# Performance work log

Hardware: AMD Instinct MI355X
Metric: run time of the kernel (lower is better)

Reference implementation:

```python
import jax, jax.numpy as jnp
import numpy as np

N_HEAD = 12
HEAD_DIM = 64
N_EMBD = 768
ATTN_MULT = 0.125
B, T = 2, 2048
NEG_INF = -1e30


def setup_inputs() -> dict:
    key = jax.random.key(0)
    ks = jax.random.split(key, 3)
    x = jax.random.normal(ks[0], (B, T, N_EMBD), dtype=jnp.float32)
    W_attn = jax.random.normal(ks[1], (N_EMBD, 3 * N_HEAD * HEAD_DIM), dtype=jnp.float32) * 0.02
    b_attn = jnp.zeros((3 * N_HEAD * HEAD_DIM,), dtype=jnp.float32)
    W_proj = jax.random.normal(ks[2], (N_HEAD * HEAD_DIM, N_EMBD), dtype=jnp.float32) * 0.02
    b_proj = jnp.zeros((N_EMBD,), dtype=jnp.float32)
    return {"x": x, "W_attn": W_attn, "b_attn": b_attn, "W_proj": W_proj, "b_proj": b_proj}


def reference(x, W_attn, b_attn, W_proj, b_proj):
    Bsz, Tlen, C = x.shape
    H, D = N_HEAD, HEAD_DIM
    qkv = x @ W_attn + b_attn                       # [B,T,3*H*D]
    q, k, v = jnp.split(qkv, 3, axis=-1)
    q = q.reshape(Bsz, Tlen, H, D).transpose(0, 2, 1, 3)   # [B,H,T,D]
    k = k.reshape(Bsz, Tlen, H, D).transpose(0, 2, 1, 3)
    v = v.reshape(Bsz, Tlen, H, D).transpose(0, 2, 1, 3)

    att = jnp.einsum('bhtd,bhsd->bhts', q, k) * ATTN_MULT  # [B,H,T,T]
    causal = jnp.tril(jnp.ones((Tlen, Tlen), dtype=bool))  # [T,T]
    att = jnp.where(causal, att, NEG_INF)

    # selection mask from head 0 (SelectionHeadLinearComboKind.NONE)
    S = jax.nn.relu(att[:, 0:1, :, :])                     # [B,1,T,T]; relu kills -inf
    # protect_bos_token: zero column 0 (key index 0)
    col = jnp.arange(Tlen)
    S = S * (col[None, None, None, :] != 0)
    # prevent_from_masking_myself: zero diagonal
    S = S * (1.0 - jnp.eye(Tlen, dtype=S.dtype))

    # accumulate selection over query (row) axis: ProtectionKind.NONE
    FF = jnp.cumsum(S, axis=-2)                            # [B,1,T,T]
    att = att - FF                                         # broadcast over heads

    p = jax.nn.softmax(att, axis=-1)                       # [B,H,T,T]
    y = jnp.einsum('bhts,bhsd->bhtd', p, v)                # [B,H,T,D]
    y = y.transpose(0, 2, 1, 3).reshape(Bsz, Tlen, H * D)  # [B,T,H*D]
    return y @ W_proj + b_proj
```

## Files before the change

### kernel.cpp

```cpp
#include <hip/hip_runtime.h>
#include <math.h>

#define T 2048
#define NH 12
#define HD 64
#define C3 2304
#define CE 768
#define NB 2

typedef __attribute__((ext_vector_type(8))) short bf16x8;
typedef __attribute__((ext_vector_type(4))) float f32x4;
typedef __attribute__((ext_vector_type(16))) float f32x16;
typedef __attribute__((ext_vector_type(4))) unsigned u32x4;

__device__ __forceinline__ void gload16(const void* g, void* l) {
    __builtin_amdgcn_global_load_lds(
        (const __attribute__((address_space(1))) void*)g,
        (__attribute__((address_space(3))) void*)l, 16, 0, 0);
}

__device__ inline void bf16split(float a, unsigned short& h, unsigned short& l) {
    unsigned int u = __float_as_uint(a);
    unsigned int r = (u + 0x7FFFu + ((u >> 16) & 1u)) >> 16;
    h = (unsigned short)r;
    float hf = __uint_as_float(r << 16);
    float lo = a - hf;
    unsigned int v = __float_as_uint(lo);
    l = (unsigned short)((v + 0x7FFFu + ((v >> 16) & 1u)) >> 16);
}

__device__ inline void packPfast(float a, float b, unsigned& wh, unsigned& wl) {
    unsigned ua = __float_as_uint(a), ub = __float_as_uint(b);
    unsigned ha = ua >> 16, hb = ub & 0xFFFF0000u;
    float la = a - __uint_as_float(ha << 16);
    float lb = b - __uint_as_float(hb);
    wh = ha | hb;
    wl = (__float_as_uint(la) >> 16) | (__float_as_uint(lb) & 0xFFFF0000u);
}

__global__ __launch_bounds__(256) void cvt_split_kernel(const float* __restrict__ A,
        unsigned short* __restrict__ H, unsigned short* __restrict__ L) {
    int i = blockIdx.x * 256 + threadIdx.x;
    float4 a0 = *(reinterpret_cast<const float4*>(A) + (size_t)i * 2);
    float4 a1 = *(reinterpret_cast<const float4*>(A) + (size_t)i * 2 + 1);
    float f[8] = {a0.x, a0.y, a0.z, a0.w, a1.x, a1.y, a1.z, a1.w};
    unsigned short h[8], l[8];
    #pragma unroll
    for (int j = 0; j < 8; ++j) bf16split(f[j], h[j], l[j]);
    uint4 hv, lv;
    hv.x = (unsigned)h[0] | ((unsigned)h[1] << 16); hv.y = (unsigned)h[2] | ((unsigned)h[3] << 16);
    hv.z = (unsigned)h[4] | ((unsigned)h[5] << 16); hv.w = (unsigned)h[6] | ((unsigned)h[7] << 16);
    lv.x = (unsigned)l[0] | ((unsigned)l[1] << 16); lv.y = (unsigned)l[2] | ((unsigned)l[3] << 16);
    lv.z = (unsigned)l[4] | ((unsigned)l[5] << 16); lv.w = (unsigned)l[6] | ((unsigned)l[7] << 16);
    reinterpret_cast<uint4*>(H)[i] = hv;
    reinterpret_cast<uint4*>(L)[i] = lv;
}

__global__ __launch_bounds__(256) void cvt_split_T_kernel(const float* __restrict__ W,
        unsigned short* __restrict__ H, unsigned short* __restrict__ L, int K, int N) {
    __shared__ float tile[64][65];
    const int n0 = blockIdx.x * 64, k0 = blockIdx.y * 64;
    const int t = threadIdx.x;
    {
        int r = t >> 2, c4 = (t & 3) * 16;
        #pragma unroll
        for (int u = 0; u < 4; ++u) {
            float4 w = *reinterpret_cast<const float4*>(&W[(size_t)(k0 + r) * N + n0 + c4 + u * 4]);
            tile[r][c4 + u * 4 + 0] = w.x; tile[r][c4 + u * 4 + 1] = w.y;
            tile[r][c4 + u * 4 + 2] = w.z; tile[r][c4 + u * 4 + 3] = w.w;
        }
    }
    __syncthreads();
    {
        int n = t >> 2, kc = (t & 3) * 16;
        unsigned short h[16], l[16];
        #pragma unroll
        for (int j = 0; j < 16; ++j) bf16split(tile[kc + j][n], h[j], l[j]);
        uint4 hv0, hv1, lv0, lv1;
        hv0.x = (unsigned)h[0] | ((unsigned)h[1] << 16);  hv0.y = (unsigned)h[2] | ((unsigned)h[3] << 16);
        hv0.z = (unsigned)h[4] | ((unsigned)h[5] << 16);  hv0.w = (unsigned)h[6] | ((unsigned)h[7] << 16);
        hv1.x = (unsigned)h[8] | ((unsigned)h[9] << 16);  hv1.y = (unsigned)h[10] | ((unsigned)h[11] << 16);
        hv1.z = (unsigned)h[12] | ((unsigned)h[13] << 16); hv1.w = (unsigned)h[14] | ((unsigned)h[15] << 16);
        lv0.x = (unsigned)l[0] | ((unsigned)l[1] << 16);  lv0.y = (unsigned)l[2] | ((unsigned)l[3] << 16);
        lv0.z = (unsigned)l[4] | ((unsigned)l[5] << 16);  lv0.w = (unsigned)l[6] | ((unsigned)l[7] << 16);
        lv1.x = (unsigned)l[8] | ((unsigned)l[9] << 16);  lv1.y = (unsigned)l[10] | ((unsigned)l[11] << 16);
        lv1.z = (unsigned)l[12] | ((unsigned)l[13] << 16); lv1.w = (unsigned)l[14] | ((unsigned)l[15] << 16);
        size_t o = (size_t)(n0 + n) * K + k0 + kc;
        reinterpret_cast<uint4*>(&H[o])[0] = hv0; reinterpret_cast<uint4*>(&H[o])[1] = hv1;
        reinterpret_cast<uint4*>(&L[o])[0] = lv0; reinterpret_cast<uint4*>(&L[o])[1] = lv1;
    }
}

__global__ __launch_bounds__(256) void cvt_kv_vt_kernel(const float* __restrict__ Vtmp,
        unsigned short* __restrict__ Vh, unsigned short* __restrict__ Vl) {
    __shared__ float tile[64][65];
    const int s0 = blockIdx.x * 64;
    const int bh = blockIdx.y;
    const int tid = threadIdx.x;
    {
        int r = tid >> 2, c0 = (tid & 3) * 16;
        const float* src = Vtmp + ((size_t)bh * T + s0 + r) * 64 + c0;
        #pragma unroll
        for (int u = 0; u < 4; ++u) {
            float4 w = *reinterpret_cast<const float4*>(src + u * 4);
            tile[r][c0 + u * 4 + 0] = w.x; tile[r][c0 + u * 4 + 1] = w.y;
            tile[r][c0 + u * 4 + 2] = w.z; tile[r][c0 + u * 4 + 3] = w.w;
        }
    }
    __syncthreads();
    {
        int d = tid >> 2, cs = (tid & 3) * 16;
        unsigned short hh[16], ll[16];
        #pragma unroll
        for (int j = 0; j < 16; ++j) bf16split(tile[cs + j][d], hh[j], ll[j]);
        uint4 hv0, hv1, lv0, lv1;
        hv0.x = (unsigned)hh[0] | ((unsigned)hh[1] << 16);  hv0.y = (unsigned)hh[2] | ((unsigned)hh[3] << 16);
        hv0.z = (unsigned)hh[4] | ((unsigned)hh[5] << 16);  hv0.w = (unsigned)hh[6] | ((unsigned)hh[7] << 16);
        hv1.x = (unsigned)hh[8] | ((unsigned)hh[9] << 16);  hv1.y = (unsigned)hh[10] | ((unsigned)hh[11] << 16);
        hv1.z = (unsigned)hh[12] | ((unsigned)hh[13] << 16); hv1.w = (unsigned)hh[14] | ((unsigned)hh[15] << 16);
        lv0.x = (unsigned)ll[0] | ((unsigned)ll[1] << 16);  lv0.y = (unsigned)ll[2] | ((unsigned)ll[3] << 16);
        lv0.z = (unsigned)ll[4] | ((unsigned)ll[5] << 16);  lv0.w = (unsigned)ll[6] | ((unsigned)ll[7] << 16);
        lv1.x = (unsigned)ll[8] | ((unsigned)ll[9] << 16);  lv1.y = (unsigned)ll[10] | ((unsigned)ll[11] << 16);
        lv1.z = (unsigned)ll[12] | ((unsigned)ll[13] << 16); lv1.w = (unsigned)ll[14] | ((unsigned)ll[15] << 16);
        size_t o = ((size_t)bh * 64 + d) * T + s0 + cs;
        reinterpret_cast<uint4*>(&Vh[o])[0] = hv0; reinterpret_cast<uint4*>(&Vh[o])[1] = hv1;
        reinterpret_cast<uint4*>(&Vl[o])[0] = lv0; reinterpret_cast<uint4*>(&Vl[o])[1] = lv1;
    }
}

#define LD32 32
__global__ __launch_bounds__(256) void gemm_mfma_kernel(
        const unsigned short* __restrict__ Ah, const unsigned short* __restrict__ Al,
        const unsigned short* __restrict__ Bh, const unsigned short* __restrict__ Bl,
        const float* __restrict__ bias, float* __restrict__ Cm,
        int M, int N, int K) {
    __shared__ unsigned short lA[2][128 * LD32];
    __shared__ unsigned short lB[2][128 * LD32];
    const int tid = threadIdx.x;
    const int nwg = gridDim.x * gridDim.y;
    int bid = blockIdx.y * gridDim.x + blockIdx.x;
    bid = (bid & 7) * (nwg >> 3) + (bid >> 3);
    const int bm = (bid / gridDim.x) * 128, bn = (bid % gridDim.x) * 128;
    const int lane = tid & 63, wid = tid >> 6;
    const int wr = wid >> 1, wc = wid & 1;
    f32x4 acc[4][4];
    #pragma unroll
    for (int i = 0; i < 4; ++i)
        #pragma unroll
        for (int j = 0; j < 4; ++j) acc[i][j] = (f32x4){0.f, 0.f, 0.f, 0.f};
    const int srow0 = wid * 32 + (lane >> 2);
    const int scn   = lane & 3;
    const int arb = wr * 64 + (lane & 15);
    const int brb = wc * 64 + (lane & 15);
    const int kc  = lane >> 4;
    for (int k0 = 0; k0 < K; k0 += 32) {
        __syncthreads();
        #pragma unroll
        for (int h = 0; h < 2; ++h) {
            int row = srow0 + h * 16;
            int cs = scn ^ ((row >> 1) & 3);
            size_t ao = (size_t)(bm + row) * K + k0 + cs * 8;
            size_t bo = (size_t)(bn + row) * K + k0 + cs * 8;
            unsigned short* d0 = &lA[0][(wid * 32 + h * 16) * LD32];
            unsigned short* d1 = &lA[1][(wid * 32 + h * 16) * LD32];
            unsigned short* d2 = &lB[0][(wid * 32 + h * 16) * LD32];
            unsigned short* d3 = &lB[1][(wid * 32 + h * 16) * LD32];
            gload16(&Ah[ao], d0);
            gload16(&Al[ao], d1);
            gload16(&Bh[bo], d2);
            gload16(&Bl[bo], d3);
        }
        __syncthreads();
        bf16x8 fa[2][4], fb[2][4];
        #pragma unroll
        for (int fi = 0; fi < 4; ++fi) {
            int ra = arb + fi * 16, rb = brb + fi * 16;
            int ca = (kc ^ ((ra >> 1) & 3)) * 8;
            int cb = (kc ^ ((rb >> 1) & 3)) * 8;
            fa[0][fi] = *reinterpret_cast<const bf16x8*>(&lA[0][ra * LD32 + ca]);
            fa[1][fi] = *reinterpret_cast<const bf16x8*>(&lA[1][ra * LD32 + ca]);
            fb[0][fi] = *reinterpret_cast<const bf16x8*>(&lB[0][rb * LD32 + cb]);
            fb[1][fi] = *reinterpret_cast<const bf16x8*>(&lB[1][rb * LD32 + cb]);
        }
        #pragma unroll
        for (int fi = 0; fi < 4; ++fi)
            #pragma unroll
            for (int fj = 0; fj < 4; ++fj) {
                acc[fi][fj] = __builtin_amdgcn_mfma_f32_16x16x32_bf16(fb[0][fj], fa[0][fi], acc[fi][fj], 0, 0, 0);
                acc[fi][fj] = __builtin_amdgcn_mfma_f32_16x16x32_bf16(fb[0][fj], fa[1][fi], acc[fi][fj], 0, 0, 0);
                acc[fi][fj] = __builtin_amdgcn_mfma_f32_16x16x32_bf16(fb[1][fj], fa[0][fi], acc[fi][fj], 0, 0, 0);
            }
    }
    const int mloc = lane & 15, ng = (lane >> 4) * 4;
    #pragma unroll
    for (int fi = 0; fi < 4; ++fi) {
        int row = bm + wr * 64 + fi * 16 + mloc;
        #pragma unroll
        for (int fj = 0; fj < 4; ++fj) {
            int n0 = bn + wc * 64 + fj * 16 + ng;
            float4 bv = *reinterpret_cast<const float4*>(&bias[n0]);
            float4 o4 = {acc[fi][fj][0] + bv.x, acc[fi][fj][1] + bv.y,
                         acc[fi][fj][2] + bv.z, acc[fi][fj][3] + bv.w};
            *reinterpret_cast<float4*>(&Cm[(size_t)row * N + n0]) = o4;
        }
    }
}

__global__ __launch_bounds__(256) void gemm_qkv_mfma_kernel(
        const unsigned short* __restrict__ Ah, const unsigned short* __restrict__ Al,
        const unsigned short* __restrict__ Bh, const unsigned short* __restrict__ Bl,
        const float* __restrict__ bias,
        unsigned short* __restrict__ Qh, unsigned short* __restrict__ Ql,
        unsigned short* __restrict__ Kh, unsigned short* __restrict__ Kl,
        float* __restrict__ Vtmp) {
    const int K = CE;
    __shared__ unsigned short lA[2][128 * LD32];
    __shared__ unsigned short lB[2][128 * LD32];
    const int tid = threadIdx.x;
    const int nwg = gridDim.x * gridDim.y;
    int bid = blockIdx.y * gridDim.x + blockIdx.x;
    bid = (bid & 7) * (nwg >> 3) + (bid >> 3);
    const int bm = (bid / gridDim.x) * 128, bn = (bid % gridDim.x) * 128;
    const int lane = tid & 63, wid = tid >> 6;
    const int wr = wid >> 1, wc = wid & 1;
    f32x4 acc[4][4];
    #pragma unroll
    for (int i = 0; i < 4; ++i)
        #pragma unroll
        for (int j = 0; j < 4; ++j) acc[i][j] = (f32x4){0.f, 0.f, 0.f, 0.f};
    const int srow0 = wid * 32 + (lane >> 2);
    const int scn   = lane & 3;
    const int arb = wr * 64 + (lane & 15);
    const int brb = wc * 64 + (lane & 15);
    const int kc  = lane >> 4;
    for (int k0 = 0; k0 < K; k0 += 32) {
        __syncthreads();
        #pragma unroll
        for (int h = 0; h < 2; ++h) {
            int row = srow0 + h * 16;
            int cs = scn ^ ((row >> 1) & 3);
            size_t ao = (size_t)(bm + row) * K + k0 + cs * 8;
            size_t bo = (size_t)(bn + row) * K + k0 + cs * 8;
            unsigned short* d0 = &lA[0][(wid * 32 + h * 16) * LD32];
            unsigned short* d1 = &lA[1][(wid * 32 + h * 16) * LD32];
            unsigned short* d2 = &lB[0][(wid * 32 + h * 16) * LD32];
            unsigned short* d3 = &lB[1][(wid * 32 + h * 16) * LD32];
            gload16(&Ah[ao], d0);
            gload16(&Al[ao], d1);
            gload16(&Bh[bo], d2);
            gload16(&Bl[bo], d3);
        }
        __syncthreads();
        bf16x8 fa[2][4], fb[2][4];
        #pragma unroll
        for (int fi = 0; fi < 4; ++fi) {
            int ra = arb + fi * 16, rb = brb + fi * 16;
            int ca = (kc ^ ((ra >> 1) & 3)) * 8;
            int cb = (kc ^ ((rb >> 1) & 3)) * 8;
            fa[0][fi] = *reinterpret_cast<const bf16x8*>(&lA[0][ra * LD32 + ca]);
            fa[1][fi] = *reinterpret_cast<const bf16x8*>(&lA[1][ra * LD32 + ca]);
            fb[0][fi] = *reinterpret_cast<const bf16x8*>(&lB[0][rb * LD32 + cb]);
            fb[1][fi] = *reinterpret_cast<const bf16x8*>(&lB[1][rb * LD32 + cb]);
        }
        #pragma unroll
        for (int fi = 0; fi < 4; ++fi)
            #pragma unroll
            for (int fj = 0; fj < 4; ++fj) {
                acc[fi][fj] = __builtin_amdgcn_mfma_f32_16x16x32_bf16(fb[0][fj], fa[0][fi], acc[fi][fj], 0, 0, 0);
                acc[fi][fj] = __builtin_amdgcn_mfma_f32_16x16x32_bf16(fb[0][fj], fa[1][fi], acc[fi][fj], 0, 0, 0);
                acc[fi][fj] = __builtin_amdgcn_mfma_f32_16x16x32_bf16(fb[1][fj], fa[0][fi], acc[fi][fj], 0, 0, 0);
            }
    }
    const int colbase = bn + wc * 64;
    const int region = colbase / 768;
    const int h = (colbase % 768) >> 6;
    const int mloc = lane & 15, ng = (lane >> 4) * 4;
    #pragma unroll
    for (int fi = 0; fi < 4; ++fi) {
        int tg = bm + wr * 64 + fi * 16 + mloc;
        int bb = tg >> 11, t = tg & (T - 1);
        #pragma unroll
        for (int fj = 0; fj < 4; ++fj) {
            int dbase = fj * 16 + ng;
            float4 bv = *reinterpret_cast<const float4*>(&bias[colbase + dbase]);
            float v0 = acc[fi][fj][0] + bv.x, v1 = acc[fi][fj][1] + bv.y;
            float v2 = acc[fi][fj][2] + bv.z, v3 = acc[fi][fj][3] + bv.w;
            size_t o = ((size_t)(bb * NH + h) * T + t) * 64 + dbase;
            if (region == 2) {
                float4 o4 = {v0, v1, v2, v3};
                *reinterpret_cast<float4*>(&Vtmp[o]) = o4;
            } else {
                unsigned short hh[4], ll[4];
                bf16split(v0, hh[0], ll[0]); bf16split(v1, hh[1], ll[1]);
                bf16split(v2, hh[2], ll[2]); bf16split(v3, hh[3], ll[3]);
                uint2 ph = {(unsigned)hh[0] | ((unsigned)hh[1] << 16),
                            (unsigned)hh[2] | ((unsigned)hh[3] << 16)};
                uint2 pl = {(unsigned)ll[0] | ((unsigned)ll[1] << 16),
                            (unsigned)ll[2] | ((unsigned)ll[3] << 16)};
                if (region == 0) {
                    *reinterpret_cast<uint2*>(&Qh[o]) = ph;
                    *reinterpret_cast<uint2*>(&Ql[o]) = pl;
                } else {
                    *reinterpret_cast<uint2*>(&Kh[o]) = ph;
                    *reinterpret_cast<uint2*>(&Kl[o]) = pl;
                }
            }
        }
    }
}

__global__ __launch_bounds__(256) void gemm_bias_kernel(
        const float* __restrict__ A, const float* __restrict__ B,
        const float* __restrict__ bias, float* __restrict__ Cm,
        int M, int N, int K) {
    __shared__ float As[16][64];
    __shared__ float Bs[16][68];
    const int tid = threadIdx.x;
    const int ty = tid >> 4, tx = tid & 15;
    const int bm = blockIdx.y * 64, bn = blockIdx.x * 64;
    float acc[4][4] = {};
    for (int k0 = 0; k0 < K; k0 += 16) {
        {
            int r = tid >> 2;
            int kk = (tid & 3) * 4;
            float4 a = *reinterpret_cast<const float4*>(&A[(size_t)(bm + r) * K + k0 + kk]);
            As[kk + 0][r] = a.x; As[kk + 1][r] = a.y; As[kk + 2][r] = a.z; As[kk + 3][r] = a.w;
        }
        {
            int kk = tid >> 4;
            int c = (tid & 15) * 4;
            *reinterpret_cast<float4*>(&Bs[kk][c]) =
                *reinterpret_cast<const float4*>(&B[(size_t)(k0 + kk) * N + bn + c]);
        }
        __syncthreads();
        #pragma unroll
        for (int kk = 0; kk < 16; ++kk) {
            float4 a4 = *reinterpret_cast<const float4*>(&As[kk][ty * 4]);
            float4 b4 = *reinterpret_cast<const float4*>(&Bs[kk][tx * 4]);
            float av[4] = {a4.x, a4.y, a4.z, a4.w};
            float bv[4] = {b4.x, b4.y, b4.z, b4.w};
            #pragma unroll
            for (int i = 0; i < 4; ++i)
                #pragma unroll
                for (int j = 0; j < 4; ++j)
                    acc[i][j] = fmaf(av[i], bv[j], acc[i][j]);
        }
        __syncthreads();
    }
    #pragma unroll
    for (int i = 0; i < 4; ++i) {
        int row = bm + ty * 4 + i;
        #pragma unroll
        for (int j = 0; j < 4; ++j) {
            int col = bn + tx * 4 + j;
            Cm[(size_t)row * N + col] = acc[i][j] + bias[col];
        }
    }
}

#define FST 72

__global__ __launch_bounds__(256) void s0_mfma_kernel(
        const unsigned short* __restrict__ Qh, const unsigned short* __restrict__ Ql,
        const unsigned short* __restrict__ Kh, const unsigned short* __restrict__ Kl,
        float* __restrict__ S, float* __restrict__ Psum) {
    const int kb = blockIdx.x * 64, qb = blockIdx.y * 64, b = blockIdx.z;
    const int tid = threadIdx.x;
    float* Sb = S + (size_t)b * T * T;
    if (kb > qb) {
        const int ty = tid >> 4, tx = tid & 15;
        #pragma unroll
        for (int i = 0; i < 4; ++i) {
            float4 z = {0.f, 0.f, 0.f, 0.f};
            *reinterpret_cast<float4*>(&Sb[(size_t)(qb + ty * 4 + i) * T + kb + tx * 4]) = z;
        }
        if (tid < 64) Psum[((size_t)(b * 32 + (qb >> 6)) * T) + kb + tid] = 0.f;
        return;
    }
    const int lane = tid & 63, w = tid >> 6;
    const int fr = lane & 15, fg = lane >> 4;
    __shared__ unsigned short Ks[2][64 * FST];
    __shared__ float csum[4][64];
    const int hb0 = b * NH;
    {
        const int sr = tid >> 2, sc0 = (tid & 3) * 16;
        const unsigned short* kh = Kh + ((size_t)hb0 * T + kb + sr) * 64 + sc0;
        const unsigned short* kl = Kl + ((size_t)hb0 * T + kb + sr) * 64 + sc0;
        uint4 a0 = reinterpret_cast<const uint4*>(kh)[0];
        uint4 a1 = reinterpret_cast<const uint4*>(kh)[1];
        uint4 b0 = reinterpret_cast<const uint4*>(kl)[0];
        uint4 b1 = reinterpret_cast<const uint4*>(kl)[1];
        *reinterpret_cast<uint4*>(&Ks[0][sr * FST + sc0 + 0]) = a0;
        *reinterpret_cast<uint4*>(&Ks[0][sr * FST + sc0 + 8]) = a1;
        *reinterpret_cast<uint4*>(&Ks[1][sr * FST + sc0 + 0]) = b0;
        *reinterpret_cast<uint4*>(&Ks[1][sr * FST + sc0 + 8]) = b1;
    }
    bf16x8 qh[2], ql[2];
    #pragma unroll
    for (int ks = 0; ks < 2; ++ks) {
        size_t qo = ((size_t)hb0 * T + qb + w * 16 + fr) * 64 + ks * 32 + fg * 8;
        qh[ks] = *reinterpret_cast<const bf16x8*>(&Qh[qo]);
        ql[ks] = *reinterpret_cast<const bf16x8*>(&Ql[qo]);
    }
    __syncthreads();
    f32x4 qk[4];
    #pragma unroll
    for (int fj = 0; fj < 4; ++fj) qk[fj] = (f32x4){0.f, 0.f, 0.f, 0.f};
    #pragma unroll
    for (int ks = 0; ks < 2; ++ks) {
        bf16x8 kbh[4], kbl[4];
        #pragma unroll
        for (int fj = 0; fj < 4; ++fj) {
            kbh[fj] = *reinterpret_cast<const bf16x8*>(&Ks[0][(fj * 16 + fr) * FST + ks * 32 + fg * 8]);
            kbl[fj] = *reinterpret_cast<const bf16x8*>(&Ks[1][(fj * 16 + fr) * FST + ks * 32 + fg * 8]);
        }
        #pragma unroll
        for (int fj = 0; fj < 4; ++fj) {
            qk[fj] = __builtin_amdgcn_mfma_f32_16x16x32_bf16(qh[ks], kbh[fj], qk[fj], 0, 0, 0);
            qk[fj] = __builtin_amdgcn_mfma_f32_16x16x32_bf16(qh[ks], kbl[fj], qk[fj], 0, 0, 0);
            qk[fj] = __builtin_amdgcn_mfma_f32_16x16x32_bf16(ql[ks], kbh[fj], qk[fj], 0, 0, 0);
        }
    }
    float colsum[4] = {0.f, 0.f, 0.f, 0.f};
    #pragma unroll
    for (int p = 0; p < 4; ++p) {
        int t = qb + w * 16 + fg * 4 + p;
        #pragma unroll
        for (int fj = 0; fj < 4; ++fj) {
            int s = kb + fj * 16 + fr;
            float v = qk[fj][p] * 0.125f;
            float o = (s >= 1 && s < t) ? fmaxf(v, 0.0f) : 0.0f;
            Sb[(size_t)t * T + s] = o;
            colsum[fj] += o;
        }
    }
    #pragma unroll
    for (int fj = 0; fj < 4; ++fj) {
        colsum[fj] += __shfl_xor(colsum[fj], 16);
        colsum[fj] += __shfl_xor(colsum[fj], 32);
    }
    if (lane < 16) {
        #pragma unroll
        for (int fj = 0; fj < 4; ++fj) csum[w][fj * 16 + lane] = colsum[fj];
    }
    __syncthreads();
    if (tid < 64) {
        float v = csum[0][tid] + csum[1][tid] + csum[2][tid] + csum[3][tid];
        Psum[((size_t)(b * 32 + (qb >> 6)) * T) + kb + tid] = v;
    }
}

__global__ __launch_bounds__(256) void s0_kernel(const float* __restrict__ qkv,
                                                 float* __restrict__ S) {
    const int kb = blockIdx.x * 64, qb = blockIdx.y * 64, b = blockIdx.z;
    const int tid = threadIdx.x, ty = tid >> 4, tx = tid & 15;
    float* Sb = S + (size_t)b * T * T;
    if (kb > qb) {
        #pragma unroll
        for (int i = 0; i < 4; ++i) {
            int row = qb + ty * 4 + i;
            float4 z = {0.f, 0.f, 0.f, 0.f};
            *reinterpret_cast<float4*>(&Sb[(size_t)row * T + kb + tx * 4]) = z;
        }
        return;
    }
    __shared__ float Qt[64][68];
    __shared__ float Kt[64][68];
    {
        int r = tid >> 2;
        int c0 = (tid & 3) * 16;
        const float* qrow = qkv + (size_t)(b * T + qb + r) * C3 + 0;
        const float* krow = qkv + (size_t)(b * T + kb + r) * C3 + 768;
        #pragma unroll
        for (int u = 0; u < 4; ++u) {
            float4 q4 = *reinterpret_cast<const float4*>(&qrow[c0 + u * 4]);
            float4 k4 = *reinterpret_cast<const float4*>(&krow[c0 + u * 4]);
            int d = c0 + u * 4;
            Qt[d + 0][r] = q4.x; Qt[d + 1][r] = q4.y; Qt[d + 2][r] = q4.z; Qt[d + 3][r] = q4.w;
            Kt[d + 0][r] = k4.x; Kt[d + 1][r] = k4.y; Kt[d + 2][r] = k4.z; Kt[d + 3][r] = k4.w;
        }
    }
    __syncthreads();
    float acc[4][4] = {};
    #pragma unroll
    for (int d = 0; d < 64; ++d) {
        float4 qv = *reinterpret_cast<const float4*>(&Qt[d][ty * 4]);
        float4 kv = *reinterpret_cast<const float4*>(&Kt[d][tx * 4]);
        float qa[4] = {qv.x, qv.y, qv.z, qv.w};
        float ka[4] = {kv.x, kv.y, kv.z, kv.w};
        #pragma unroll
        for (int i = 0; i < 4; ++i)
            #pragma unroll
            for (int j = 0; j < 4; ++j)
                acc[i][j] = fmaf(qa[i], ka[j], acc[i][j]);
    }
    #pragma unroll
    for (int i = 0; i < 4; ++i) {
        int t = qb + ty * 4 + i;
        float o[4];
        #pragma unroll
        for (int j = 0; j < 4; ++j) {
            int s = kb + tx * 4 + j;
            float v = acc[i][j] * 0.125f;
            o[j] = (s >= 1 && s < t) ? fmaxf(v, 0.0f) : 0.0f;
        }
        float4 o4 = {o[0], o[1], o[2], o[3]};
        *reinterpret_cast<float4*>(&Sb[(size_t)t * T + kb + tx * 4]) = o4;
    }
}

__global__ __launch_bounds__(256) void colsum_kernel(const float* __restrict__ S,
                                                     float* __restrict__ Psum) {
    int s = blockIdx.x * 256 + threadIdx.x;
    int j = blockIdx.y, b = blockIdx.z;
    const float* Sb = S + (size_t)b * T * T;
    float sum = 0.f;
    for (int r = 0; r < 64; ++r) sum += Sb[(size_t)(j * 64 + r) * T + s];
    Psum[((size_t)b * 32 + j) * T + s] = sum;
}

__global__ __launch_bounds__(256) void scanseg_kernel(float* __restrict__ Psum) {
    int s = blockIdx.x * 256 + threadIdx.x;
    int b = blockIdx.y;
    float v[32];
    #pragma unroll
    for (int j = 0; j < 32; ++j)
        v[j] = Psum[((size_t)(b * 32 + j)) * T + s];
    float run = 0.f;
    #pragma unroll
    for (int j = 0; j < 32; ++j) {
        Psum[((size_t)(b * 32 + j)) * T + s] = run;
        run += v[j];
    }
}

__global__ __launch_bounds__(256) void ffscan_kernel(float* __restrict__ S,
                                                     const float* __restrict__ Psum) {
    int s = blockIdx.x * 256 + threadIdx.x;
    int j = blockIdx.y, b = blockIdx.z;
    float run = Psum[((size_t)b * 32 + j) * T + s];
    float* Sb = S + (size_t)b * T * T;
    for (int r0 = 0; r0 < 64; r0 += 8) {
        float v[8];
        #pragma unroll
        for (int i = 0; i < 8; ++i)
            v[i] = Sb[(size_t)(j * 64 + r0 + i) * T + s];
        #pragma unroll
        for (int i = 0; i < 8; ++i) {
            run += v[i];
            Sb[(size_t)(j * 64 + r0 + i) * T + s] = run;
        }
    }
}

__device__ const int FTQ[40] = {15,15,15,15,14,14,14,13,13,13,12,12,12,11,11,11,10,10,9,9,8,8,7,7,6,5,4,3,14,10,6,2,13,9,5,1,12,8,4,0};
__device__ const int FK0[40] = {0,8,16,24,0,8,16,0,8,16,0,8,16,0,8,16,0,8,0,8,0,8,0,8,0,0,0,0,24,16,8,0,24,16,8,0,24,16,8,0};
__device__ const int FK1[40] = {8,16,24,32,8,16,24,8,16,24,8,16,24,8,16,24,8,16,8,16,8,16,8,16,8,8,8,8,30,22,14,6,28,20,12,4,26,18,10,2};
__device__ const int FCB[12] = {0,2,4,6,8,11,14,17,20,24,28,32};

__global__ __launch_bounds__(256) void flash_mfma_kernel(
        const unsigned short* __restrict__ Qh, const unsigned short* __restrict__ Ql,
        const unsigned short* __restrict__ Kh, const unsigned short* __restrict__ Kl,
        const unsigned short* __restrict__ Vth, const unsigned short* __restrict__ Vtl,
        const float* __restrict__ FF,
        unsigned short* __restrict__ Yh, unsigned short* __restrict__ Yl,
        float* __restrict__ PART) {
    int g = blockIdx.y * gridDim.x + blockIdx.x;
    const int hb = (g & 7) * 3 + ((g >> 3) % 3);
    const int u  = (g >> 3) / 3;
    const int h = hb % NH, b = hb / NH;
    const int tq = FTQ[u], kt0 = FK0[u], kt1 = FK1[u];
    const int qb = tq * 128;
    const int tid = threadIdx.x;
    const int lane = tid & 63, w = tid >> 6;
    const int q31 = lane & 31, hi = lane >> 5;
    const int trow = qb + w * 32 + q31;
    __shared__ unsigned short KS[2][64 * FST];
    __shared__ unsigned short VS[2][64 * FST];

    bf16x8 qfh[4], qfl[4];
    #pragma unroll
    for (int dblk = 0; dblk < 4; ++dblk) {
        size_t qo = ((size_t)hb * T + trow) * 64 + dblk * 16 + hi * 8;
        qfh[dblk] = *reinterpret_cast<const bf16x8*>(&Qh[qo]);
        qfl[dblk] = *reinterpret_cast<const bf16x8*>(&Ql[qo]);
    }

    f32x16 oacc0 = (f32x16)(0.f), oacc1 = (f32x16)(0.f);
    float m = -1e30f, l = 0.f;
    const float* FFb = FF + (size_t)b * T * T;
    const int sr = tid >> 2, sc0 = (tid & 3) * 16;

    {
        const int kb = kt0 * 64;
        const unsigned short* ksrc = Kh + ((size_t)hb * T + kb + sr) * 64 + sc0;
        const unsigned short* ksrl = Kl + ((size_t)hb * T + kb + sr) * 64 + sc0;
        const unsigned short* vsrc = Vth + ((size_t)hb * 64 + sr) * T + kb + sc0;
        const unsigned short* vsrl = Vtl + ((size_t)hb * 64 + sr) * T + kb + sc0;
        uint4 a0 = reinterpret_cast<const uint4*>(ksrc)[0];
        uint4 a1 = reinterpret_cast<const uint4*>(ksrc)[1];
        uint4 a2 = reinterpret_cast<const uint4*>(ksrl)[0];
        uint4 a3 = reinterpret_cast<const uint4*>(ksrl)[1];
        uint4 a4 = reinterpret_cast<const uint4*>(vsrc)[0];
        uint4 a5 = reinterpret_cast<const uint4*>(vsrc)[1];
        uint4 a6 = reinterpret_cast<const uint4*>(vsrl)[0];
        uint4 a7 = reinterpret_cast<const uint4*>(vsrl)[1];
        *reinterpret_cast<uint4*>(&KS[0][sr * FST + sc0 + 0]) = a0;
        *reinterpret_cast<uint4*>(&KS[0][sr * FST + sc0 + 8]) = a1;
        *reinterpret_cast<uint4*>(&KS[1][sr * FST + sc0 + 0]) = a2;
        *reinterpret_cast<uint4*>(&KS[1][sr * FST + sc0 + 8]) = a3;
        *reinterpret_cast<uint4*>(&VS[0][sr * FST + sc0 + 0]) = a4;
        *reinterpret_cast<uint4*>(&VS[0][sr * FST + sc0 + 8]) = a5;
        *reinterpret_cast<uint4*>(&VS[1][sr * FST + sc0 + 0]) = a6;
        *reinterpret_cast<uint4*>(&VS[1][sr * FST + sc0 + 8]) = a7;
    }
    __syncthreads();

    for (int kt = kt0; kt < kt1; ++kt) {
        const int kb = kt * 64;
        const bool has_next = (kt + 1 < kt1);
        uint4 p0, p1, p2, p3, p4, p5, p6, p7;
        if (has_next) {
            const int kb2 = kb + 64;
            const unsigned short* ksrc = Kh + ((size_t)hb * T + kb2 + sr) * 64 + sc0;
            const unsigned short* ksrl = Kl + ((size_t)hb * T + kb2 + sr) * 64 + sc0;
            const unsigned short* vsrc = Vth + ((size_t)hb * 64 + sr) * T + kb2 + sc0;
            const unsigned short* vsrl = Vtl + ((size_t)hb * 64 + sr) * T + kb2 + sc0;
            p0 = reinterpret_cast<const uint4*>(ksrc)[0];
            p1 = reinterpret_cast<const uint4*>(ksrc)[1];
            p2 = reinterpret_cast<const uint4*>(ksrl)[0];
            p3 = reinterpret_cast<const uint4*>(ksrl)[1];
            p4 = reinterpret_cast<const uint4*>(vsrc)[0];
            p5 = reinterpret_cast<const uint4*>(vsrc)[1];
            p6 = reinterpret_cast<const uint4*>(vsrl)[0];
            p7 = reinterpret_cast<const uint4*>(vsrl)[1];
        }
        f32x16 acc0 = (f32x16)(0.f), acc1 = (f32x16)(0.f);
        #pragma unroll
        for (int dblk = 0; dblk < 4; ++dblk) {
            bf16x8 kfh = *reinterpret_cast<const bf16x8*>(&KS[0][(q31) * FST + dblk * 16 + hi * 8]);
            bf16x8 kfl = *reinterpret_cast<const bf16x8*>(&KS[1][(q31) * FST + dblk * 16 + hi * 8]);
            acc0 = __builtin_amdgcn_mfma_f32_32x32x16_bf16(kfh, qfh[dblk], acc0, 0, 0, 0);
            acc0 = __builtin_amdgcn_mfma_f32_32x32x16_bf16(kfh, qfl[dblk], acc0, 0, 0, 0);
            acc0 = __builtin_amdgcn_mfma_f32_32x32x16_bf16(kfl, qfh[dblk], acc0, 0, 0, 0);
        }
        float4 ffv[2][4];
        #pragma unroll
        for (int sb = 0; sb < 2; ++sb)
            #pragma unroll
            for (int gg = 0; gg < 4; ++gg)
                ffv[sb][gg] = *reinterpret_cast<const float4*>(
                    &FFb[(size_t)trow * T + kb + sb * 32 + gg * 8 + hi * 4]);
        #pragma unroll
        for (int dblk = 0; dblk < 4; ++dblk) {
            bf16x8 kfh = *reinterpret_cast<const bf16x8*>(&KS[0][(32 + q31) * FST + dblk * 16 + hi * 8]);
            bf16x8 kfl = *reinterpret_cast<const bf16x8*>(&KS[1][(32 + q31) * FST + dblk * 16 + hi * 8]);
            acc1 = __builtin_amdgcn_mfma_f32_32x32x16_bf16(kfh, qfh[dblk], acc1, 0, 0, 0);
            acc1 = __builtin_amdgcn_mfma_f32_32x32x16_bf16(kfh, qfl[dblk], acc1, 0, 0, 0);
            acc1 = __builtin_amdgcn_mfma_f32_32x32x16_bf16(kfl, qfh[dblk], acc1, 0, 0, 0);
        }
        float pv[2][16];
        #pragma unroll
        for (int gg = 0; gg < 4; ++gg) {
            float fv0[4] = {ffv[0][gg].x, ffv[0][gg].y, ffv[0][gg].z, ffv[0][gg].w};
            float fv1[4] = {ffv[1][gg].x, ffv[1][gg].y, ffv[1][gg].z, ffv[1][gg].w};
            #pragma unroll
            for (int a = 0; a < 4; ++a) {
                int r = gg * 4 + a;
                int s0i = kb + a + gg * 8 + hi * 4;
                int s1i = s0i + 32;
                float v0 = acc0[r] * 0.125f - fv0[a];
                float v1 = acc1[r] * 0.125f - fv1[a];
                pv[0][r] = (s0i <= trow) ? v0 : -1e30f;
                pv[1][r] = (s1i <= trow) ? v1 : -1e30f;
            }
        }
        float tm = pv[0][0];
        #pragma unroll
        for (int sb = 0; sb < 2; ++sb)
            #pragma unroll
            for (int r = 0; r < 16; ++r) tm = fmaxf(tm, pv[sb][r]);
        tm = fmaxf(tm, __shfl_xor(tm, 32));
        float mn = fmaxf(m, tm);
        float scale = __expf(m - mn);
        float rs = 0.f;
        #pragma unroll
        for (int sb = 0; sb < 2; ++sb)
            #pragma unroll
            for (int r = 0; r < 16; ++r) {
                float pe = __expf(pv[sb][r] - mn);
                pv[sb][r] = pe; rs += pe;
            }
        rs += __shfl_xor(rs, 32);
        l = l * scale + rs;
        m = mn;
        oacc0 *= scale; oacc1 *= scale;
        unsigned wh[2][4][2], wl[2][4][2];
        #pragma unroll
        for (int sb = 0; sb < 2; ++sb)
            #pragma unroll
            for (int bq = 0; bq < 4; ++bq)
                #pragma unroll
                for (int h2 = 0; h2 < 2; ++h2)
                    packPfast(pv[sb][4 * bq + 2 * h2], pv[sb][4 * bq + 2 * h2 + 1],
                              wh[sb][bq][h2], wl[sb][bq][h2]);
        #pragma unroll
        for (int kk = 0; kk < 4; ++kk) {
            const int sb = kk >> 1;
            const int b0 = 2 * (kk & 1), b1 = b0 + 1;
            unsigned sh_b1_0 = (unsigned)__shfl_xor((int)wh[sb][b1][0], 32);
            unsigned sh_b1_1 = (unsigned)__shfl_xor((int)wh[sb][b1][1], 32);
            unsigned sh_b0_0 = (unsigned)__shfl_xor((int)wh[sb][b0][0], 32);
            unsigned sh_b0_1 = (unsigned)__shfl_xor((int)wh[sb][b0][1], 32);
            unsigned sl_b1_0 = (unsigned)__shfl_xor((int)wl[sb][b1][0], 32);
            unsigned sl_b1_1 = (unsigned)__shfl_xor((int)wl[sb][b1][1], 32);
            unsigned sl_b0_0 = (unsigned)__shfl_xor((int)wl[sb][b0][0], 32);
            unsigned sl_b0_1 = (unsigned)__shfl_xor((int)wl[sb][b0][1], 32);
            u32x4 th, tl;
            th[0] = hi ? sh_b1_0 : wh[sb][b0][0];
            th[1] = hi ? sh_b1_1 : wh[sb][b0][1];
            th[2] = hi ? wh[sb][b1][0] : sh_b0_0;
            th[3] = hi ? wh[sb][b1][1] : sh_b0_1;
            tl[0] = hi ? sl_b1_0 : wl[sb][b0][0];
            tl[1] = hi ? sl_b1_1 : wl[sb][b0][1];
            tl[2] = hi ? wl[sb][b1][0] : sl_b0_0;
            tl[3] = hi ? wl[sb][b1][1] : sl_b0_1;
            bf16x8 pbh = __builtin_bit_cast(bf16x8, th);
            bf16x8 pbl = __builtin_bit_cast(bf16x8, tl);
            {
                bf16x8 vfh = *reinterpret_cast<const bf16x8*>(&VS[0][(q31) * FST + kk * 16 + hi * 8]);
                bf16x8 vfl = *reinterpret_cast<const bf16x8*>(&VS[1][(q31) * FST + kk * 16 + hi * 8]);
                oacc0 = __builtin_amdgcn_mfma_f32_32x32x16_bf16(vfh, pbh, oacc0, 0, 0, 0);
                oacc0 = __builtin_amdgcn_mfma_f32_32x32x16_bf16(vfh, pbl, oacc0, 0, 0, 0);
                oacc0 = __builtin_amdgcn_mfma_f32_32x32x16_bf16(vfl, pbh, oacc0, 0, 0, 0);
            }
            {
                bf16x8 vfh = *reinterpret_cast<const bf16x8*>(&VS[0][(32 + q31) * FST + kk * 16 + hi * 8]);
                bf16x8 vfl = *reinterpret_cast<const bf16x8*>(&VS[1][(32 + q31) * FST + kk * 16 + hi * 8]);
                oacc1 = __builtin_amdgcn_mfma_f32_32x32x16_bf16(vfh, pbh, oacc1, 0, 0, 0);
                oacc1 = __builtin_amdgcn_mfma_f32_32x32x16_bf16(vfh, pbl, oacc1, 0, 0, 0);
                oacc1 = __builtin_amdgcn_mfma_f32_32x32x16_bf16(vfl, pbh, oacc1, 0, 0, 0);
            }
        }
        __syncthreads();
        if (has_next) {
            *reinterpret_cast<uint4*>(&KS[0][sr * FST + sc0 + 0]) = p0;
            *reinterpret_cast<uint4*>(&KS[0][sr * FST + sc0 + 8]) = p1;
            *reinterpret_cast<uint4*>(&KS[1][sr * FST + sc0 + 0]) = p2;
            *reinterpret_cast<uint4*>(&KS[1][sr * FST + sc0 + 8]) = p3;
            *reinterpret_cast<uint4*>(&VS[0][sr * FST + sc0 + 0]) = p4;
            *reinterpret_cast<uint4*>(&VS[0][sr * FST + sc0 + 8]) = p5;
            *reinterpret_cast<uint4*>(&VS[1][sr * FST + sc0 + 0]) = p6;
            *reinterpret_cast<uint4*>(&VS[1][sr * FST + sc0 + 8]) = p7;
        }
        __syncthreads();
    }
    if (tq < 4) {
        float inv = 1.f / l;
        size_t ybase = ((size_t)(b * T + trow)) * CE + h * 64;
        #pragma unroll
        for (int gg = 0; gg < 4; ++gg) {
            unsigned short h0[4], l0[4], h1[4], l1[4];
            #pragma unroll
            for (int i = 0; i < 4; ++i) {
                bf16split(oacc0[4 * gg + i] * inv, h0[i], l0[i]);
                bf16split(oacc1[4 * gg + i] * inv, h1[i], l1[i]);
            }
            uint2 ph0 = {(unsigned)h0[0] | ((unsigned)h0[1] << 16), (unsigned)h0[2] | ((unsigned)h0[3] << 16)};
            uint2 pl0 = {(unsigned)l0[0] | ((unsigned)l0[1] << 16), (unsigned)l0[2] | ((unsigned)l0[3] << 16)};
            uint2 ph1 = {(unsigned)h1[0] | ((unsigned)h1[1] << 16), (unsigned)h1[2] | ((unsigned)h1[3] << 16)};
            uint2 pl1 = {(unsigned)l1[0] | ((unsigned)l1[1] << 16), (unsigned)l1[2] | ((unsigned)l1[3] << 16)};
            *reinterpret_cast<uint2*>(&Yh[ybase + gg * 8 + hi * 4]) = ph0;
            *reinterpret_cast<uint2*>(&Yl[ybase + gg * 8 + hi * 4]) = pl0;
            *reinterpret_cast<uint2*>(&Yh[ybase + 32 + gg * 8 + hi * 4]) = ph1;
            *reinterpret_cast<uint2*>(&Yl[ybase + 32 + gg * 8 + hi * 4]) = pl1;
        }
    } else {
        const int ci = FCB[tq - 4] + (kt0 >> 3);
        float* Ob = PART + (size_t)(hb * 36 + ci) * 8448;
        const int rr = w * 32 + q31;
        #pragma unroll
        for (int gg = 0; gg < 4; ++gg) {
            float4 o0 = {oacc0[4 * gg + 0], oacc0[4 * gg + 1], oacc0[4 * gg + 2], oacc0[4 * gg + 3]};
            float4 o1 = {oacc1[4 * gg + 0], oacc1[4 * gg + 1], oacc1[4 * gg + 2], oacc1[4 * gg + 3]};
            *reinterpret_cast<float4*>(&Ob[rr * 64 + gg * 8 + hi * 4]) = o0;
            *reinterpret_cast<float4*>(&Ob[rr * 64 + 32 + gg * 8 + hi * 4]) = o1;
        }
        if (hi == 0) { Ob[8192 + rr] = m; Ob[8192 + 128 + rr] = l; }
    }
}

__global__ __launch_bounds__(256) void merge128_kernel(const float* __restrict__ PART,
                                                       unsigned short* __restrict__ Yh,
                                                       unsigned short* __restrict__ Yl) {
    const int hb = blockIdx.x;
    const int tq = 4 + blockIdx.y;
    const int h = hb % NH, b = hb / NH;
    const int nch = (tq >= 12) ? 4 : (tq >= 8) ? 3 : 2;
    const float* base = PART + (size_t)(hb * 36 + FCB[tq - 4]) * 8448;
    const int tid = threadIdx.x;
    const int r = tid >> 1, half = tid & 1;
    float mm[4], la[4];
    float M = -1e30f;
    #pragma unroll
    for (int c = 0; c < 4; ++c) {
        int cc = (c < nch) ? c : 0;
        float mv = base[(size_t)cc * 8448 + 8192 + r];
        float lv = base[(size_t)cc * 8448 + 8192 + 128 + r];
        mm[c] = (c < nch) ? mv : -1e30f;
        la[c] = (c < nch) ? lv : 0.f;
        M = fmaxf(M, mm[c]);
    }
    float a[4], L = 0.f;
    #pragma unroll
    for (int c = 0; c < 4; ++c) {
        a[c] = (c < nch) ? __expf(mm[c] - M) : 0.f;
        L += a[c] * la[c];
    }
    float inv = 1.f / L;
    const int t = tq * 128 + r;
    size_t ybase = ((size_t)(b * T + t)) * CE + h * 64 + half * 32;
    #pragma unroll
    for (int uu = 0; uu < 8; ++uu) {
        float ax = 0.f, ay = 0.f, az = 0.f, aw = 0.f;
        #pragma unroll
        for (int c = 0; c < 4; ++c) {
            int cc = (c < nch) ? c : 0;
            float4 x = *reinterpret_cast<const float4*>(
                &base[(size_t)cc * 8448 + r * 64 + half * 32 + uu * 4]);
            ax += a[c] * x.x; ay += a[c] * x.y; az += a[c] * x.z; aw += a[c] * x.w;
        }
        unsigned short hh[4], ll[4];
        bf16split(ax * inv, hh[0], ll[0]); bf16split(ay * inv, hh[1], ll[1]);
        bf16split(az * inv, hh[2], ll[2]); bf16split(aw * inv, hh[3], ll[3]);
        uint2 ph = {(unsigned)hh[0] | ((unsigned)hh[1] << 16), (unsigned)hh[2] | ((unsigned)hh[3] << 16)};
        uint2 pl = {(unsigned)ll[0] | ((unsigned)ll[1] << 16), (unsigned)ll[2] | ((unsigned)ll[3] << 16)};
        *reinterpret_cast<uint2*>(&Yh[ybase + uu * 4]) = ph;
        *reinterpret_cast<uint2*>(&Yl[ybase + uu * 4]) = pl;
    }
}

__global__ __launch_bounds__(256) void flash_kernel(const float* __restrict__ qkv,
                                                    const float* __restrict__ FF,
                                                    float* __restrict__ Y,
                                                    float* __restrict__ PO,
                                                    float* __restrict__ PML,
                                                    int split) {
    const int hb = blockIdx.x;
    const int h = hb % NH, b = hb / NH;
    int qt, kt0, kt1, mode;
    if (split) {
        const int u = blockIdx.y;
        if (u < 16)      { qt = 16 + u; kt0 = 0;  kt1 = 16;     mode = 1; }
        else if (u < 32) { qt = 31 - u; kt0 = 0;  kt1 = qt + 1; mode = 0; }
        else             { qt = 63 - u; kt0 = 16; kt1 = qt + 1; mode = 2; }
    } else {
        qt = 31 - blockIdx.y; kt0 = 0; kt1 = qt + 1; mode = 0;
    }
    const int qb = qt * 64;
    const int tid = threadIdx.x, ty = tid >> 4, tx = tid & 15;
    __shared__ float Qt[64][68];
    __shared__ float KtPs[64][68];
    __shared__ float Vs[64][68];
    const int r = tid >> 2, c0 = (tid & 3) * 16;
    {
        const float* qrow = qkv + (size_t)(b * T + qb + r) * C3 + h * 64;
        #pragma unroll
        for (int u = 0; u < 4; ++u) {
            float4 q4 = *reinterpret_cast<const float4*>(&qrow[c0 + u * 4]);
            int d = c0 + u * 4;
            Qt[d + 0][r] = q4.x; Qt[d + 1][r] = q4.y; Qt[d + 2][r] = q4.z; Qt[d + 3][r] = q4.w;
        }
    }
    float m[4], l[4], O[4][4];
    #pragma unroll
    for (int i = 0; i < 4; ++i) {
        m[i] = -1e30f; l[i] = 0.f;
        #pragma unroll
        for (int j = 0; j < 4; ++j) O[i][j] = 0.f;
    }
    const float* FFb = FF + (size_t)b * T * T;
    for (int kt = kt0; kt < kt1; ++kt) {
        const int kb = kt * 64;
        __syncthreads();
        {
            const float* krow = qkv + (size_t)(b * T + kb + r) * C3 + 768 + h * 64;
            const float* vrow = qkv + (size_t)(b * T + kb + r) * C3 + 1536 + h * 64;
            #pragma unroll
            for (int u = 0; u < 4; ++u) {
                float4 k4 = *reinterpret_cast<const float4*>(&krow[c0 + u * 4]);
                int d = c0 + u * 4;
                KtPs[d + 0][r] = k4.x; KtPs[d + 1][r] = k4.y;
                KtPs[d + 2][r] = k4.z; KtPs[d + 3][r] = k4.w;
                *reinterpret_cast<float4*>(&Vs[r][c0 + u * 4]) =
                    *reinterpret_cast<const float4*>(&vrow[c0 + u * 4]);
            }
        }
        __syncthreads();
        float sc[4][4] = {};
        #pragma unroll
        for (int d = 0; d < 64; ++d) {
            float4 qv = *reinterpret_cast<const float4*>(&Qt[d][ty * 4]);
            float4 kv = *reinterpret_cast<const float4*>(&KtPs[d][tx * 4]);
            float qa[4] = {qv.x, qv.y, qv.z, qv.w};
            float ka[4] = {kv.x, kv.y, kv.z, kv.w};
            #pragma unroll
            for (int i = 0; i < 4; ++i)
                #pragma unroll
                for (int j = 0; j < 4; ++j)
                    sc[i][j] = fmaf(qa[i], ka[j], sc[i][j]);
        }
        #pragma unroll
        for (int i = 0; i < 4; ++i) {
            int t = qb + ty * 4 + i;
            float4 f4 = *reinterpret_cast<const float4*>(&FFb[(size_t)t * T + kb + tx * 4]);
            float fv[4] = {f4.x, f4.y, f4.z, f4.w};
            #pragma unroll
            for (int j = 0; j < 4; ++j) {
                int s = kb + tx * 4 + j;
                float v = sc[i][j] * 0.125f - fv[j];
                sc[i][j] = (s <= t) ? v : -1e30f;
            }
        }
        #pragma unroll
        for (int i = 0; i < 4; ++i) {
            float tm = fmaxf(fmaxf(sc[i][0], sc[i][1]), fmaxf(sc[i][2], sc[i][3]));
            tm = fmaxf(tm, __shfl_xor(tm, 1));
            tm = fmaxf(tm, __shfl_xor(tm, 2));
            tm = fmaxf(tm, __shfl_xor(tm, 4));
            tm = fmaxf(tm, __shfl_xor(tm, 8));
            float mn = fmaxf(m[i], tm);
            float scale = __expf(m[i] - mn);
            float rs = 0.f;
            #pragma unroll
            for (int j = 0; j < 4; ++j) {
                float p = __expf(sc[i][j] - mn);
                sc[i][j] = p; rs += p;
            }
            rs += __shfl_xor(rs, 1); rs += __shfl_xor(rs, 2);
            rs += __shfl_xor(rs, 4); rs += __shfl_xor(rs, 8);
            l[i] = l[i] * scale + rs;
            m[i] = mn;
            #pragma unroll
            for (int j = 0; j < 4; ++j) O[i][j] *= scale;
        }
        __syncthreads();
        #pragma unroll
        for (int i = 0; i < 4; ++i) {
            float4 p4 = {sc[i][0], sc[i][1], sc[i][2], sc[i][3]};
            *reinterpret_cast<float4*>(&KtPs[ty * 4 + i][tx * 4]) = p4;
        }
        __syncthreads();
        #pragma unroll
        for (int j4 = 0; j4 < 16; ++j4) {
            float pvv[4][4];
            #pragma unroll
            for (int i = 0; i < 4; ++i) {
                float4 t4 = *reinterpret_cast<const float4*>(&KtPs[ty * 4 + i][j4 * 4]);
                pvv[i][0] = t4.x; pvv[i][1] = t4.y; pvv[i][2] = t4.z; pvv[i][3] = t4.w;
            }
            #pragma unroll
            for (int jj = 0; jj < 4; ++jj) {
                float4 v4 = *reinterpret_cast<const float4*>(&Vs[j4 * 4 + jj][tx * 4]);
                float vv[4] = {v4.x, v4.y, v4.z, v4.w};
                #pragma unroll
                for (int i = 0; i < 4; ++i)
                    #pragma unroll
                    for (int dd = 0; dd < 4; ++dd)
                        O[i][dd] = fmaf(pvv[i][jj], vv[dd], O[i][dd]);
            }
        }
    }
    if (mode == 0) {
        #pragma unroll
        for (int i = 0; i < 4; ++i) {
            int t = qb + ty * 4 + i;
            float inv = 1.f / l[i];
            float4 o4 = {O[i][0] * inv, O[i][1] * inv, O[i][2] * inv, O[i][3] * inv};
            *reinterpret_cast<float4*>(&Y[(size_t)(b * T + t) * CE + h * 64 + tx * 4]) = o4;
        }
    } else {
        const int pidx = (b * NH + h) * 16 + (qt - 16);
        float* Ob  = PO  + (size_t)(mode - 1) * (NB * NH * 16 * 4096) + (size_t)pidx * 4096;
        float* mlb = PML + (size_t)(mode - 1) * (NB * NH * 16 * 128)  + (size_t)pidx * 128;
        #pragma unroll
        for (int i = 0; i < 4; ++i) {
            int rr = ty * 4 + i;
            float4 o4 = {O[i][0], O[i][1], O[i][2], O[i][3]};
            *reinterpret_cast<float4*>(&Ob[rr * 64 + tx * 4]) = o4;
            if (tx == 0) { mlb[rr] = m[i]; mlb[64 + rr] = l[i]; }
        }
    }
}

__global__ __launch_bounds__(256) void merge_kernel(const float* __restrict__ PO,
                                                    const float* __restrict__ PML,
                                                    float* __restrict__ Y) {
    const int p = blockIdx.x;
    const int q16 = p & 15;
// ... 132 lines not shown
```

Measured before the change: 247.3 us.

## Stage Q/K epilogue through LDS for coalesced stores; lazy softmax rescale

The QKV GEMM epilogue for the Q and K regions now writes the bf16 high and low halves into swizzled LDS scratch (reusing the A/B tiles) and then writes them out as 16-byte coalesced rows, instead of scattered 8-byte stores per fragment. The attention kernel skips the running-max rescale of the output accumulators when the whole wave's new tile max stays within 8 of the current max. This trades extra barriers and LDS traffic for fewer global store transactions, and trades some exp headroom (values up to e^8) for fewer multiplies on most iterations.

```diff
diff --git a/kernel.cpp b/kernel.cpp
--- a/kernel.cpp
+++ b/kernel.cpp
@@ -271,40 +271,99 @@
                 acc[fi][fj] = __builtin_amdgcn_mfma_f32_16x16x32_bf16(fb[1][fj], fa[0][fi], acc[fi][fj], 0, 0, 0);
             }
     }
-    const int colbase = bn + wc * 64;
-    const int region = colbase / 768;
-    const int h = (colbase % 768) >> 6;
+    const int region = bn / 768;
     const int mloc = lane & 15, ng = (lane >> 4) * 4;
-    #pragma unroll
-    for (int fi = 0; fi < 4; ++fi) {
-        int tg = bm + wr * 64 + fi * 16 + mloc;
-        int bb = tg >> 11, t = tg & (T - 1);
-        #pragma unroll
-        for (int fj = 0; fj < 4; ++fj) {
-            int dbase = fj * 16 + ng;
-            float4 bv = *reinterpret_cast<const float4*>(&bias[colbase + dbase]);
-            float v0 = acc[fi][fj][0] + bv.x, v1 = acc[fi][fj][1] + bv.y;
-            float v2 = acc[fi][fj][2] + bv.z, v3 = acc[fi][fj][3] + bv.w;
-            size_t o = ((size_t)(bb * NH + h) * T + t) * 64 + dbase;
-            if (region == 2) {
-                float4 o4 = {v0, v1, v2, v3};
+    if (region == 2) {
+        const int colbase = bn + wc * 64;
+        const int h = (colbase % 768) >> 6;
+        #pragma unroll
+        for (int fi = 0; fi < 4; ++fi) {
+            int tg = bm + wr * 64 + fi * 16 + mloc;
+            int bb = tg >> 11, t = tg & (T - 1);
+            #pragma unroll
+            for (int fj = 0; fj < 4; ++fj) {
+                int dbase = fj * 16 + ng;
+                float4 bv = *reinterpret_cast<const float4*>(&bias[colbase + dbase]);
+                float4 o4 = {acc[fi][fj][0] + bv.x, acc[fi][fj][1] + bv.y,
+                             acc[fi][fj][2] + bv.z, acc[fi][fj][3] + bv.w};
+                size_t o = ((size_t)(bb * NH + h) * T + t) * 64 + dbase;
                 *reinterpret_cast<float4*>(&Vtmp[o]) = o4;
-            } else {
-                unsigned short hh[4], ll[4];
-                bf16split(v0, hh[0], ll[0]); bf16split(v1, hh[1], ll[1]);
-                bf16split(v2, hh[2], ll[2]); bf16split(v3, hh[3], ll[3]);
-                uint2 ph = {(unsigned)hh[0] | ((unsigned)hh[1] << 16),
-                            (unsigned)hh[2] | ((unsigned)hh[3] << 16)};
-                uint2 pl = {(unsigned)ll[0] | ((unsigned)ll[1] << 16),
-                            (unsigned)ll[2] | ((unsigned)ll[3] << 16)};
-                if (region == 0) {
-                    *reinterpret_cast<uint2*>(&Qh[o]) = ph;
-                    *reinterpret_cast<uint2*>(&Ql[o]) = pl;
-                } else {
-                    *reinterpret_cast<uint2*>(&Kh[o]) = ph;
-                    *reinterpret_cast<uint2*>(&Kl[o]) = pl;
+            }
+        }
+    } else {
+        unsigned short* dstH = (region == 0) ? Qh : Kh;
+        unsigned short* dstL = (region == 0) ? Ql : Kl;
+        unsigned lo0[16], lo1[16];
+        __syncthreads();
+        {
+            unsigned short* SCR = (wr == 0) ? &lA[0][0] : &lB[0][0];
+            #pragma unroll
+            for (int fi = 0; fi < 4; ++fi) {
+                int tloc = wr * 64 + fi * 16 + mloc;
+                int rin = tloc & 63;
+                #pragma unroll
+                for (int fj = 0; fj < 4; ++fj) {
+                    int clocw = wc * 64 + fj * 16 + ng;
+                    float4 bv = *reinterpret_cast<const float4*>(&bias[bn + clocw]);
+                    unsigned short hh[4], ll[4];
+                    bf16split(acc[fi][fj][0] + bv.x, hh[0], ll[0]);
+                    bf16split(acc[fi][fj][1] + bv.y, hh[1], ll[1]);
+                    bf16split(acc[fi][fj][2] + bv.z, hh[2], ll[2]);
+                    bf16split(acc[fi][fj][3] + bv.w, hh[3], ll[3]);
+                    int unit = clocw >> 3;
+                    int po = rin * 128 + ((unit ^ (tloc & 7)) << 3) + (clocw & 7);
+                    uint2 ph = {(unsigned)hh[0] | ((unsigned)hh[1] << 16),
+                                (unsigned)hh[2] | ((unsigned)hh[3] << 16)};
+                    *reinterpret_cast<uint2*>(&SCR[po]) = ph;
+                    lo0[fi * 4 + fj] = (unsigned)ll[0] | ((unsigned)ll[1] << 16);
+                    lo1[fi * 4 + fj] = (unsigned)ll[2] | ((unsigned)ll[3] << 16);
                 }
             }
+        }
+        __syncthreads();
+        #pragma unroll
+        for (int it = 0; it < 8; ++it) {
+            int idx = it * 256 + tid;
+            int tloc = idx >> 4;
+            int unit = idx & 15;
+            unsigned short* SCR = (tloc < 64) ? &lA[0][0] : &lB[0][0];
+            int rin = tloc & 63;
+            uint4 v = *reinterpret_cast<uint4*>(&SCR[rin * 128 + ((unit ^ (tloc & 7)) << 3)]);
+            int tg = bm + tloc; int bb = tg >> 11; int t = tg & (T - 1);
+            int cl = unit << 3;
+            int hh2 = ((bn + cl) % 768) >> 6;
+            *reinterpret_cast<uint4*>(&dstH[((size_t)(bb * NH + hh2) * T + t) * 64 + (cl & 63)]) = v;
+        }
+        __syncthreads();
+        {
+            unsigned short* SCR = (wr == 0) ? &lA[0][0] : &lB[0][0];
+            #pragma unroll
+            for (int fi = 0; fi < 4; ++fi) {
+                int tloc = wr * 64 + fi * 16 + mloc;
+                int rin = tloc & 63;
+                #pragma unroll
+                for (int fj = 0; fj < 4; ++fj) {
+                    int clocw = wc * 64 + fj * 16 + ng;
+                    int unit = clocw >> 3;
+                    int po = rin * 128 + ((unit ^ (tloc & 7)) << 3) + (clocw & 7);
+                    uint2 pl = {lo0[fi * 4 + fj], lo1[fi * 4 + fj]};
+                    *reinterpret_cast<uint2*>(&SCR[po]) = pl;
+                }
+            }
+        }
+        __syncthreads();
+        #pragma unroll
+        for (int it = 0; it < 8; ++it) {
+            int idx = it * 256 + tid;
+            int tloc = idx >> 4;
+            int unit = idx & 15;
+            unsigned short* SCR = (tloc < 64) ? &lA[0][0] : &lB[0][0];
+            int rin = tloc & 63;
+            uint4 v = *reinterpret_cast<uint4*>(&SCR[rin * 128 + ((unit ^ (tloc & 7)) << 3)]);
+            int tg = bm + tloc; int bb = tg >> 11; int t = tg & (T - 1);
+            int cl = unit << 3;
+            int hh2 = ((bn + cl) % 768) >> 6;
+            *reinterpret_cast<uint4*>(&dstL[((size_t)(bb * NH + hh2) * T + t) * 64 + (cl & 63)]) = v;
         }
     }
 }
@@ -681,20 +740,23 @@
             #pragma unroll
             for (int r = 0; r < 16; ++r) tm = fmaxf(tm, pv[sb][r]);
         tm = fmaxf(tm, __shfl_xor(tm, 32));
-        float mn = fmaxf(m, tm);
-        float scale = __expf(m - mn);
+        if (!__all(tm <= m + 8.0f)) {
+            float mn = fmaxf(m, tm);
+            float scale = __expf(m - mn);
+            l *= scale;
+            oacc0 *= scale; oacc1 *= scale;
+            m = mn;
+        }
         float rs = 0.f;
         #pragma unroll
         for (int sb = 0; sb < 2; ++sb)
             #pragma unroll
             for (int r = 0; r < 16; ++r) {
-                float pe = __expf(pv[sb][r] - mn);
+                float pe = __expf(pv[sb][r] - m);
                 pv[sb][r] = pe; rs += pe;
             }
         rs += __shfl_xor(rs, 32);
-        l = l * scale + rs;
-        m = mn;
-        oacc0 *= scale; oacc1 *= scale;
+        l += rs;
         unsigned wh[2][4][2], wl[2][4][2];
         #pragma unroll
         for (int sb = 0; sb < 2; ++sb)
```

Measured after the change: 268.3 us. 8.5% more time.
